# Performance work log

Hardware: AMD Instinct MI355X
Metric: run time of the kernel (lower is better)

## Reference

```python
import jax, jax.numpy as jnp
import numpy as np

B, L, D, K, NRBF = 2, 2048, 128, 3, 16
NUM_ATOMS = 118


def setup_inputs() -> dict:
    key = jax.random.key(0)
    ks = jax.random.split(key, 20)
    s = 0.05
    inp = {
        "coords": jax.random.normal(ks[0], (B, L, 3), dtype=jnp.float32) * 3.0,
        "Z": jax.random.randint(ks[1], (B, L), 0, NUM_ATOMS),
        # CoordEncoder params
        "atom_emb": jax.random.normal(ks[2], (NUM_ATOMS, D), dtype=jnp.float32) * s,
        "gamma": jnp.asarray(10.0, dtype=jnp.float32),
        "rbf_centers": jnp.linspace(0.0, 5.0, NRBF, dtype=jnp.float32),
        "rbf_w": jax.random.normal(ks[3], (NRBF, D), dtype=jnp.float32) * s,
        "rbf_b": jnp.zeros((D,), dtype=jnp.float32),
        "out_w": jax.random.normal(ks[4], (2 * D, D), dtype=jnp.float32) * s,
        "out_b": jnp.zeros((D,), dtype=jnp.float32),
        # MP_Layer params, stacked over K layers
        "self_w": jax.random.normal(ks[5], (K, D, D), dtype=jnp.float32) * s,
        "self_b": jnp.zeros((K, D), dtype=jnp.float32),
        "msg_w": jax.random.normal(ks[6], (K, D, D), dtype=jnp.float32) * s,
        "msg_b": jnp.zeros((K, D), dtype=jnp.float32),
        "upd_w": jax.random.normal(ks[7], (K, 2 * D, D), dtype=jnp.float32) * s,
        "upd_b": jnp.zeros((K, D), dtype=jnp.float32),
    }
    return inp


def _pairwise_dist(coords):
    # coords: [B,L,3] -> dist: [B,L,L]; safe sqrt so diagonal has zero grad
    diff = coords[:, :, None, :] - coords[:, None, :, :]
    sq = jnp.sum(diff * diff, axis=-1)
    return jnp.where(sq > 0, jnp.sqrt(jnp.where(sq > 0, sq, 1.0)), 0.0)


def reference(coords, Z, atom_emb, gamma, rbf_centers, rbf_w, rbf_b,
              out_w, out_b, self_w, self_b, msg_w, msg_b, upd_w, upd_b):
    # --- CoordEncoder ---
    h_atom = atom_emb[Z]                                   # [B,L,D]
    dist = _pairwise_dist(coords)                          # [B,L,L]
    rbf = jnp.exp(-gamma * (dist[..., None] - rbf_centers) ** 2)  # [B,L,L,R]
    rbf_local = rbf.mean(axis=2)                           # [B,L,R]
    h_geo = rbf_local @ rbf_w + rbf_b                      # [B,L,D]
    h = jnp.concatenate([h_atom, h_geo], axis=-1) @ out_w + out_b  # [B,L,D]
    # --- MP layers (mask is None; W = exp(-dist) is the same every layer) ---
    W = jnp.exp(-dist)                                     # [B,L,L]
    for k in range(K):
        msg = jnp.einsum("bij,bjd->bid", W, h @ msg_w[k] + msg_b[k])
        h = jnp.concatenate([h @ self_w[k] + self_b[k], msg], axis=-1) @ upd_w[k] + upd_b[k]
    return h
```

## Files before the change

### kernel.cpp

```cpp
#include <hip/hip_runtime.h>
#include <hip/hip_bf16.h>

typedef unsigned short u16;
typedef __bf16 bf16x8 __attribute__((ext_vector_type(8)));
typedef float f32x4 __attribute__((ext_vector_type(4)));
typedef u16 u16x4 __attribute__((ext_vector_type(4)));

#define B_ 2
#define L_ 2048
#define D_ 128
#define KLAY 3
#define NR 16
#define DD (D_ * D_)
#define XTN (L_ * D_)
#define NFOLD 6

static __device__ __forceinline__ u16 f2bf(float f) {
    union { float f; unsigned u; } v; v.f = f;
    unsigned r = v.u + 0x7FFFu + ((v.u >> 16) & 1u);
    return (u16)(r >> 16);
}
static __device__ __forceinline__ bf16x8 ld_bf8(const u16* p) {
    return *(const bf16x8*)p;
}

__global__ __launch_bounds__(1024) void enc_kernel(
    const float* coords, const int* Z, const float* atom_emb,
    const float* gamma_p, const float* centers, const float* rbf_w,
    const float* rbf_b, const float* out_w, const float* out_b,
    const float* self_w, const float* self_b, const float* msg_w,
    const float* msg_b, const float* upd_w, const float* upd_b,
    u16* h_rm, u16* hT, float* rowsum,
    u16* foldA, u16* foldB, float* c0v, float* cvv) {
    int bid = blockIdx.x;
    int tid = threadIdx.x;
    int w = tid >> 6, lane = tid & 63;
    int rowf = lane & 15, kg = lane >> 4;
    __shared__ __align__(16) char smem[34816];
    f32x4 z = {0.f, 0.f, 0.f, 0.f};

    if (bid < NFOLD) {
        int lay = bid >> 1, mat = bid & 1;
        const float* Wsrc = (mat ? msg_w : self_w) + lay * DD;
        const float* U = upd_w + lay * 2 * DD + mat * DD;
        u16* dst = (mat ? foldB : foldA) + lay * DD;
        u16(*A_l)[68] = (u16(*)[68])smem;
        u16(*BT_l)[68] = (u16(*)[68])(smem + 17408);
        f32x4 acc[4] = {z, z, z, z};
        int ncol = (w & 7) * 16 + rowf;
        int rfh = w >> 3;
        for (int half = 0; half < 2; half++) {
            int m0 = half * 64;
            for (int o = tid; o < 128 * 64; o += 1024) {
                int kk = o >> 6, mm = o & 63;
                A_l[kk][mm] = f2bf(Wsrc[kk * D_ + m0 + mm]);
            }
            for (int o = tid; o < 128 * 64; o += 1024) {
                int nn = o >> 6, mm = o & 63;
                BT_l[nn][mm] = f2bf(U[(m0 + mm) * D_ + nn]);
            }
            __syncthreads();
#pragma unroll
            for (int rfi = 0; rfi < 4; rfi++) {
                int rf = rfh * 4 + rfi;
#pragma unroll
                for (int ks = 0; ks < 2; ks++) {
                    int k0 = ks * 32 + kg * 8;
                    acc[rfi] = __builtin_amdgcn_mfma_f32_16x16x32_bf16(
                        ld_bf8(&A_l[rf * 16 + rowf][k0]),
                        ld_bf8(&BT_l[ncol][k0]), acc[rfi], 0, 0, 0);
                }
            }
            __syncthreads();
        }
#pragma unroll
        for (int rfi = 0; rfi < 4; rfi++) {
            int rf = rfh * 4 + rfi;
            u16x4 pk;
#pragma unroll
            for (int r = 0; r < 4; r++) pk[r] = f2bf(acc[rfi][r]);
            *(u16x4*)&dst[ncol * D_ + rf * 16 + kg * 4] = pk;
        }
        if (tid < D_) {
            const float* bsrc = (mat ? msg_b : self_b) + lay * D_;
            float s = 0.f;
            for (int m = 0; m < D_; m++) s += bsrc[m] * U[m * D_ + tid];
            if (mat == 0) c0v[lay * D_ + tid] = s + upd_b[lay * D_ + tid];
            else cvv[lay * D_ + tid] = s;
        }
        return;
    }

    int rt = bid - NFOLD;
    int gi0 = rt * 16;
    int b = gi0 >> 11;
    int il0 = gi0 & (L_ - 1);
    float* cj = (float*)smem;
    u16* hgeo = (u16*)(smem + 24576);
    float* rbf_l = (float*)(smem + 24576 + 4352);

    for (int i = tid; i < 1536; i += 1024)
        ((float4*)cj)[i] = ((const float4*)(coords + (size_t)b * L_ * 3))[i];
    __syncthreads();

    {
        int row = tid >> 6, s6 = tid & 63;
        float gamma = gamma_p[0];
        float dl = centers[1] - centers[0];
        float c4[4];
#pragma unroll
        for (int g = 0; g < 4; g++) c4[g] = centers[4 * g];
        float two_gdl = 2.f * gamma * dl;
        float cx = cj[(il0 + row) * 3 + 0];
        float cy = cj[(il0 + row) * 3 + 1];
        float cz = cj[(il0 + row) * 3 + 2];
        float acc[4][4];
#pragma unroll
        for (int g = 0; g < 4; g++)
#pragma unroll
            for (int m = 0; m < 4; m++) acc[g][m] = 0.f;
        float wsum = 0.f;
        for (int it = 0; it < 32; it++) {
            int j = s6 + 64 * it;
            float dx = cx - cj[j * 3 + 0];
            float dy = cy - cj[j * 3 + 1];
            float dz = cz - cj[j * 3 + 2];
            float sq = dx * dx + dy * dy + dz * dz;
            float d = sqrtf(sq);
            wsum += __expf(-d);
#pragma unroll
            for (int g = 0; g < 4; g++) {
                float x = d - c4[g];
                float base = __expf(-gamma * x * x);
                float u = __expf(fminf(two_gdl * x, 29.f));
                float p = base;
                acc[g][0] += p;
                p *= u; acc[g][1] += p;
                p *= u; acc[g][2] += p;
                p *= u; acc[g][3] += p;
            }
        }
#pragma unroll
        for (int off = 32; off > 0; off >>= 1) {
            wsum += __shfl_xor(wsum, off);
#pragma unroll
            for (int g = 0; g < 4; g++)
#pragma unroll
                for (int m = 0; m < 4; m++) acc[g][m] += __shfl_xor(acc[g][m], off);
        }
        if (s6 == 0) {
            rowsum[gi0 + row] = wsum;
#pragma unroll
            for (int m = 0; m < 4; m++) {
                float Km = __expf(-gamma * (m * dl) * (m * dl)) * (1.0f / L_);
#pragma unroll
                for (int g = 0; g < 4; g++)
                    rbf_l[row * NR + 4 * g + m] = acc[g][m] * Km;
            }
        }
    }
    __syncthreads();

    for (int e = tid; e < 16 * D_; e += 1024) {
        int row = e >> 7, d = e & 127;
        float s = rbf_b[d];
#pragma unroll
        for (int r = 0; r < NR; r++) s += rbf_l[row * NR + r] * rbf_w[r * D_ + d];
        hgeo[row * 136 + d] = f2bf(s);
    }
    __syncthreads();

    if (w < 8) {
        f32x4 a1 = z;
        int za = Z[gi0 + rowf];
        int cl = w * 16 + rowf;
#pragma unroll
        for (int ks = 0; ks < 8; ks++) {
            int k0 = ks * 32 + kg * 8;
            bf16x8 av;
            if (k0 < 128) {
                union { bf16x8 v; u16 e[8]; } t;
                const float* ap = atom_emb + (size_t)za * D_ + k0;
#pragma unroll
                for (int e = 0; e < 8; e++) t.e[e] = f2bf(ap[e]);
                av = t.v;
            } else {
                av = ld_bf8(hgeo + rowf * 136 + (k0 - 128));
            }
            union { bf16x8 v; u16 e[8]; } bv;
            const float* bp = out_w + (size_t)k0 * D_ + cl;
#pragma unroll
            for (int e = 0; e < 8; e++) bv.e[e] = f2bf(bp[e * D_]);
            a1 = __builtin_amdgcn_mfma_f32_16x16x32_bf16(av, bv.v, a1, 0, 0, 0);
        }
        float bias = out_b[cl];
        u16x4 pk;
#pragma unroll
        for (int r = 0; r < 4; r++) pk[r] = f2bf(a1[r] + bias);
#pragma unroll
        for (int r = 0; r < 4; r++)
            h_rm[(size_t)(gi0 + kg * 4 + r) * D_ + cl] = pk[r];
        *(u16x4*)&hT[(size_t)b * XTN + ((il0 + kg * 4) >> 5) * (32 * D_) + cl * 32 +
                     ((il0 + kg * 4) & 31)] = pk;
    }
}

__global__ __launch_bounds__(1024) void mp_kernel(
    const float* coords, const u16* h_in, const u16* hT_in, const float* rowsum,
    const u16* foldA_k, const u16* foldB_k, const float* c0_k, const float* cv_k,
    u16* h_out, u16* hT_out, float* out_f32, int last) {
    int rt = blockIdx.x;
    int gi0 = rt * 16;
    int b = gi0 >> 11;
    int il0 = gi0 & (L_ - 1);
    int tid = threadIdx.x;
    int w = tid >> 6, lane = tid & 63;
    int rowf = lane & 15, kg = lane >> 4;

    __shared__ __align__(16) float cj[L_ * 3];
    __shared__ __align__(16) float red[4][16][128];
    u16* g_lds = (u16*)&red[0][0][0];

    for (int i = tid; i < 1536; i += 1024)
        ((float4*)cj)[i] = ((const float4*)(coords + (size_t)b * L_ * 3))[i];
    __syncthreads();

    float rx = cj[(il0 + rowf) * 3 + 0];
    float ry = cj[(il0 + rowf) * 3 + 1];
    float rz = cj[(il0 + rowf) * 3 + 2];

    f32x4 z = {0.f, 0.f, 0.f, 0.f};
    f32x4 acc[8] = {z, z, z, z, z, z, z, z};
    const u16* xbase = hT_in + (size_t)b * XTN + (w * 4) * (32 * D_) + rowf * 32 + kg * 8;
#pragma unroll
    for (int s = 0; s < 4; s++) {
        int j0 = w * 128 + s * 32 + kg * 8;
        union { bf16x8 v; __bf16 e[8]; } wf;
#pragma unroll
        for (int e = 0; e < 8; e++) {
            int jl = j0 + e;
            float dx = rx - cj[jl * 3 + 0];
            float dy = ry - cj[jl * 3 + 1];
            float dz = rz - cj[jl * 3 + 2];
            float sq = dx * dx + dy * dy + dz * dz;
            float d = sq > 0.f ? sqrtf(sq) : 0.f;
            wf.e[e] = (__bf16)__expf(-d);
        }
#pragma unroll
        for (int n = 0; n < 8; n++) {
            bf16x8 bb = ld_bf8(xbase + s * (32 * D_) + n * 512);
            acc[n] = __builtin_amdgcn_mfma_f32_16x16x32_bf16(wf.v, bb, acc[n], 0, 0, 0);
        }
    }
    auto stash = [&](int slot) {
#pragma unroll
        for (int n = 0; n < 8; n++)
#pragma unroll
            for (int r = 0; r < 4; r++) {
                int row = kg * 4 + r, col = n * 16 + rowf;
                red[slot][row][(col + 4 * row) & 127] = acc[n][r];
            }
    };
    auto grab = [&](int slot) {
#pragma unroll
        for (int n = 0; n < 8; n++)
#pragma unroll
            for (int r = 0; r < 4; r++) {
                int row = kg * 4 + r, col = n * 16 + rowf;
                acc[n][r] += red[slot][row][(col + 4 * row) & 127];
            }
    };
    if (w >= 8 && w < 12) stash(w - 8);
    __syncthreads();
    if (w < 4) grab(w);
    __syncthreads();
    if (w >= 12) stash(w - 12);
    __syncthreads();
    if (w >= 4 && w < 8) grab(w - 4);
    __syncthreads();
    if (w >= 4 && w < 8) stash(w - 4);
    __syncthreads();
    if (w < 4) grab(w);
    if (w == 2 || w == 3) stash(w);
    __syncthreads();
    if (w < 2) grab(w + 2);
    if (w == 1) stash(3);
    __syncthreads();
    if (w == 0) {
        grab(3);
#pragma unroll
        for (int n = 0; n < 8; n++)
#pragma unroll
            for (int r = 0; r < 4; r++)
                g_lds[(kg * 4 + r) * 136 + n * 16 + rowf] = f2bf(acc[n][r]);
    }
    __syncthreads();

    if (w < 8) {
        f32x4 acc2 = z;
        int cl = w * 16 + rowf;
#pragma unroll
        for (int ks = 0; ks < 4; ks++) {
            int k0 = ks * 32 + kg * 8;
            bf16x8 ah = ld_bf8(h_in + (size_t)(gi0 + rowf) * D_ + k0);
            acc2 = __builtin_amdgcn_mfma_f32_16x16x32_bf16(
                ah, ld_bf8(foldA_k + cl * D_ + k0), acc2, 0, 0, 0);
            bf16x8 ag = ld_bf8(g_lds + rowf * 136 + k0);
            acc2 = __builtin_amdgcn_mfma_f32_16x16x32_bf16(
                ag, ld_bf8(foldB_k + cl * D_ + k0), acc2, 0, 0, 0);
        }
        float c0 = c0_k[cl], cv = cv_k[cl];
        if (last) {
#pragma unroll
            for (int r = 0; r < 4; r++) {
                int row = kg * 4 + r;
                out_f32[(size_t)(gi0 + row) * D_ + cl] =
                    acc2[r] + c0 + rowsum[gi0 + row] * cv;
            }
        } else {
#pragma unroll
            for (int r = 0; r < 4; r++) {
                int row = kg * 4 + r;
                float val = acc2[r] + c0 + rowsum[gi0 + row] * cv;
                u16 hv = f2bf(val);
                h_out[(size_t)(gi0 + row) * D_ + cl] = hv;
                int jj = il0 + row;
                hT_out[(size_t)b * XTN + (jj >> 5) * (32 * D_) + cl * 32 + (jj & 31)] = hv;
            }
        }
    }
}

extern "C" void kernel_launch(void* const* d_in, const int* in_sizes, int n_in,
                              void* d_out, int out_size, void* d_ws, size_t ws_size,
                              hipStream_t stream) {
    const float* coords = (const float*)d_in[0];
    const int* Z = (const int*)d_in[1];
    const float* atom_emb = (const float*)d_in[2];
    const float* gamma = (const float*)d_in[3];
    const float* centers = (const float*)d_in[4];
    const float* rbf_w = (const float*)d_in[5];
    const float* rbf_b = (const float*)d_in[6];
    const float* out_w = (const float*)d_in[7];
    const float* out_b = (const float*)d_in[8];
    const float* self_w = (const float*)d_in[9];
    const float* self_b = (const float*)d_in[10];
    const float* msg_w = (const float*)d_in[11];
    const float* msg_b = (const float*)d_in[12];
    const float* upd_w = (const float*)d_in[13];
    const float* upd_b = (const float*)d_in[14];
    float* out = (float*)d_out;

    char* ws = (char*)d_ws;
    u16* h_a = (u16*)(ws + 0);
    u16* h_b = (u16*)(ws + 1048576);
    u16* hT_a = (u16*)(ws + 2097152);
    u16* hT_b = (u16*)(ws + 3145728);
    float* rowsum = (float*)(ws + 4194304);
    u16* foldA = (u16*)(ws + 4210688);
    u16* foldB = (u16*)(ws + 4308992);
    float* c0v = (float*)(ws + 4407296);
    float* cvv = (float*)(ws + 4408832);

    enc_kernel<<<256 + NFOLD, 1024, 0, stream>>>(
        coords, Z, atom_emb, gamma, centers, rbf_w, rbf_b, out_w, out_b,
        self_w, self_b, msg_w, msg_b, upd_w, upd_b,
        h_a, hT_a, rowsum, foldA, foldB, c0v, cvv);
    mp_kernel<<<256, 1024, 0, stream>>>(
        coords, h_a, hT_a, rowsum, foldA + 0 * DD, foldB + 0 * DD,
        c0v + 0 * D_, cvv + 0 * D_, h_b, hT_b, out, 0);
    mp_kernel<<<256, 1024, 0, stream>>>(
        coords, h_b, hT_b, rowsum, foldA + 1 * DD, foldB + 1 * DD,
        c0v + 1 * D_, cvv + 1 * D_, h_a, hT_a, out, 0);
    mp_kernel<<<256, 1024, 0, stream>>>(
        coords, h_a, hT_a, rowsum, foldA + 2 * DD, foldB + 2 * DD,
        c0v + 2 * D_, cvv + 2 * D_, h_b, hT_b, out, 1);
}
```

Baseline: 109.2 us.

## Split encoder into pairwise partial-sum kernel and finalize kernel with j-split

The fused encoder kernel becomes two kernels. The first computes pairwise RBF and exp(-d) partial sums, with each 16-row tile's j-range split into 4 quarter blocks (1024 blocks of 512 threads). The second reduces the partials and runs the rbf_w and out_w projections. The aim is more parallelism and occupancy for the dominant pairwise stage, which had only 256 large blocks. The cost is an extra launch plus a global-memory round trip for the partial sums. The weight-fold blocks also change to 512 threads, each computing 8 output tiles.

```diff
diff --git a/kernel.cpp b/kernel.cpp
--- a/kernel.cpp
+++ b/kernel.cpp
@@ -13,6 +13,8 @@
 #define NR 16
 #define DD (D_ * D_)
 #define XTN (L_ * D_)
+#define BL (B_ * L_)
+#define BLN (BL * NR)
 #define NFOLD 6
 
 static __device__ __forceinline__ u16 f2bf(float f) {
@@ -24,62 +26,55 @@
     return *(const bf16x8*)p;
 }
 
-__global__ __launch_bounds__(1024) void enc_kernel(
-    const float* coords, const int* Z, const float* atom_emb,
-    const float* gamma_p, const float* centers, const float* rbf_w,
-    const float* rbf_b, const float* out_w, const float* out_b,
-    const float* self_w, const float* self_b, const float* msg_w,
-    const float* msg_b, const float* upd_w, const float* upd_b,
-    u16* h_rm, u16* hT, float* rowsum,
-    u16* foldA, u16* foldB, float* c0v, float* cvv) {
+__global__ __launch_bounds__(512) void pairw_kernel(
+    const float* coords, const float* gamma_p, const float* centers,
+    const float* self_w, const float* msg_w, const float* upd_w,
+    const float* self_b, const float* msg_b, const float* upd_b,
+    float* rbfp, float* rsp, u16* foldA, u16* foldB, float* c0v, float* cvv) {
     int bid = blockIdx.x;
     int tid = threadIdx.x;
-    int w = tid >> 6, lane = tid & 63;
-    int rowf = lane & 15, kg = lane >> 4;
     __shared__ __align__(16) char smem[34816];
     f32x4 z = {0.f, 0.f, 0.f, 0.f};
 
     if (bid < NFOLD) {
+        int w = tid >> 6, lane = tid & 63;
+        int rowf = lane & 15, kg = lane >> 4;
         int lay = bid >> 1, mat = bid & 1;
         const float* Wsrc = (mat ? msg_w : self_w) + lay * DD;
         const float* U = upd_w + lay * 2 * DD + mat * DD;
         u16* dst = (mat ? foldB : foldA) + lay * DD;
         u16(*A_l)[68] = (u16(*)[68])smem;
         u16(*BT_l)[68] = (u16(*)[68])(smem + 17408);
-        f32x4 acc[4] = {z, z, z, z};
-        int ncol = (w & 7) * 16 + rowf;
-        int rfh = w >> 3;
+        f32x4 acc[8] = {z, z, z, z, z, z, z, z};
         for (int half = 0; half < 2; half++) {
             int m0 = half * 64;
-            for (int o = tid; o < 128 * 64; o += 1024) {
+            for (int o = tid; o < 128 * 64; o += 512) {
                 int kk = o >> 6, mm = o & 63;
                 A_l[kk][mm] = f2bf(Wsrc[kk * D_ + m0 + mm]);
             }
-            for (int o = tid; o < 128 * 64; o += 1024) {
+            for (int o = tid; o < 128 * 64; o += 512) {
                 int nn = o >> 6, mm = o & 63;
                 BT_l[nn][mm] = f2bf(U[(m0 + mm) * D_ + nn]);
             }
             __syncthreads();
 #pragma unroll
-            for (int rfi = 0; rfi < 4; rfi++) {
-                int rf = rfh * 4 + rfi;
+            for (int rf = 0; rf < 8; rf++)
 #pragma unroll
                 for (int ks = 0; ks < 2; ks++) {
                     int k0 = ks * 32 + kg * 8;
-                    acc[rfi] = __builtin_amdgcn_mfma_f32_16x16x32_bf16(
+                    acc[rf] = __builtin_amdgcn_mfma_f32_16x16x32_bf16(
                         ld_bf8(&A_l[rf * 16 + rowf][k0]),
-                        ld_bf8(&BT_l[ncol][k0]), acc[rfi], 0, 0, 0);
+                        ld_bf8(&BT_l[w * 16 + rowf][k0]), acc[rf], 0, 0, 0);
                 }
-            }
             __syncthreads();
         }
-#pragma unroll
-        for (int rfi = 0; rfi < 4; rfi++) {
-            int rf = rfh * 4 + rfi;
+        int n = w * 16 + rowf;
+#pragma unroll
+        for (int rf = 0; rf < 8; rf++) {
             u16x4 pk;
 #pragma unroll
-            for (int r = 0; r < 4; r++) pk[r] = f2bf(acc[rfi][r]);
-            *(u16x4*)&dst[ncol * D_ + rf * 16 + kg * 4] = pk;
+            for (int r = 0; r < 4; r++) pk[r] = f2bf(acc[rf][r]);
+            *(u16x4*)&dst[n * D_ + rf * 16 + kg * 4] = pk;
         }
         if (tid < D_) {
             const float* bsrc = (mat ? msg_b : self_b) + lay * D_;
@@ -91,89 +86,117 @@
         return;
     }
 
-    int rt = bid - NFOLD;
+    int rt = (bid - NFOLD) >> 2, jq = (bid - NFOLD) & 3;
     int gi0 = rt * 16;
     int b = gi0 >> 11;
+    int row = tid >> 5, s5 = tid & 31;
+    int gi = gi0 + row;
+    float* cj = (float*)smem;
+    {
+        const float4* src = (const float4*)(coords + ((size_t)b * L_ + jq * 512) * 3);
+        if (tid < 384) ((float4*)cj)[tid] = src[tid];
+    }
+    float gamma = gamma_p[0];
+    float dl = centers[1] - centers[0];
+    float c4[4];
+#pragma unroll
+    for (int g = 0; g < 4; g++) c4[g] = centers[4 * g];
+    float two_gdl = 2.f * gamma * dl;
+    float cx = coords[gi * 3 + 0];
+    float cy = coords[gi * 3 + 1];
+    float cz = coords[gi * 3 + 2];
+    __syncthreads();
+
+    float acc[4][4];
+#pragma unroll
+    for (int g = 0; g < 4; g++)
+#pragma unroll
+        for (int m = 0; m < 4; m++) acc[g][m] = 0.f;
+    float wsum = 0.f;
+#pragma unroll 4
+    for (int it = 0; it < 16; it++) {
+        int jl = s5 + 32 * it;
+        float dx = cx - cj[jl * 3 + 0];
+        float dy = cy - cj[jl * 3 + 1];
+        float dz = cz - cj[jl * 3 + 2];
+        float sq = dx * dx + dy * dy + dz * dz;
+        float d = sqrtf(sq);
+        wsum += __expf(-d);
+#pragma unroll
+        for (int g = 0; g < 4; g++) {
+            float x = d - c4[g];
+            float base = __expf(-gamma * x * x);
+            float u1 = __expf(fminf(two_gdl * x, 29.f));
+            float u2 = u1 * u1;
+            acc[g][0] += base;
+            acc[g][1] += base * u1;
+            acc[g][2] += base * u2;
+            acc[g][3] += base * (u2 * u1);
+        }
+    }
+#pragma unroll
+    for (int off = 16; off > 0; off >>= 1) {
+        wsum += __shfl_xor(wsum, off);
+#pragma unroll
+        for (int g = 0; g < 4; g++)
+#pragma unroll
+            for (int m = 0; m < 4; m++) acc[g][m] += __shfl_xor(acc[g][m], off);
+    }
+    if (s5 == 0) {
+        rsp[(size_t)jq * BL + gi] = wsum;
+#pragma unroll
+        for (int m = 0; m < 4; m++) {
+            float Km = __expf(-gamma * (m * dl) * (m * dl)) * (1.0f / L_);
+#pragma unroll
+            for (int g = 0; g < 4; g++)
+                rbfp[(size_t)jq * BLN + (size_t)gi * NR + 4 * g + m] = acc[g][m] * Km;
+        }
+    }
+}
+
+__global__ __launch_bounds__(256) void encf_kernel(
+    const int* Z, const float* atom_emb, const float* rbf_w, const float* rbf_b,
+    const float* out_w, const float* out_b, const float* rbfp, const float* rsp,
+    u16* h_rm, u16* hT, float* rowsum) {
+    int gi0 = blockIdx.x * 16;
+    int b = gi0 >> 11;
     int il0 = gi0 & (L_ - 1);
-    float* cj = (float*)smem;
-    u16* hgeo = (u16*)(smem + 24576);
-    float* rbf_l = (float*)(smem + 24576 + 4352);
-
-    for (int i = tid; i < 1536; i += 1024)
-        ((float4*)cj)[i] = ((const float4*)(coords + (size_t)b * L_ * 3))[i];
-    __syncthreads();
+    int tid = threadIdx.x;
+    int w = tid >> 6, lane = tid & 63;
+    int rowf = lane & 15, kg = lane >> 4;
+    __shared__ float rbf_lds[16][NR];
+    __shared__ __align__(16) u16 hgeo[16][136];
 
     {
-        int row = tid >> 6, s6 = tid & 63;
-        float gamma = gamma_p[0];
-        float dl = centers[1] - centers[0];
-        float c4[4];
-#pragma unroll
-        for (int g = 0; g < 4; g++) c4[g] = centers[4 * g];
-        float two_gdl = 2.f * gamma * dl;
-        float cx = cj[(il0 + row) * 3 + 0];
-        float cy = cj[(il0 + row) * 3 + 1];
-        float cz = cj[(il0 + row) * 3 + 2];
-        float acc[4][4];
-#pragma unroll
-        for (int g = 0; g < 4; g++)
-#pragma unroll
-            for (int m = 0; m < 4; m++) acc[g][m] = 0.f;
-        float wsum = 0.f;
-        for (int it = 0; it < 32; it++) {
-            int j = s6 + 64 * it;
-            float dx = cx - cj[j * 3 + 0];
-            float dy = cy - cj[j * 3 + 1];
-            float dz = cz - cj[j * 3 + 2];
-            float sq = dx * dx + dy * dy + dz * dz;
-            float d = sqrtf(sq);
-            wsum += __expf(-d);
-#pragma unroll
-            for (int g = 0; g < 4; g++) {
-                float x = d - c4[g];
-                float base = __expf(-gamma * x * x);
-                float u = __expf(fminf(two_gdl * x, 29.f));
-                float p = base;
-                acc[g][0] += p;
-                p *= u; acc[g][1] += p;
-                p *= u; acc[g][2] += p;
-                p *= u; acc[g][3] += p;
-            }
-        }
-#pragma unroll
-        for (int off = 32; off > 0; off >>= 1) {
-            wsum += __shfl_xor(wsum, off);
-#pragma unroll
-            for (int g = 0; g < 4; g++)
-#pragma unroll
-                for (int m = 0; m < 4; m++) acc[g][m] += __shfl_xor(acc[g][m], off);
-        }
-        if (s6 == 0) {
-            rowsum[gi0 + row] = wsum;
-#pragma unroll
-            for (int m = 0; m < 4; m++) {
-                float Km = __expf(-gamma * (m * dl) * (m * dl)) * (1.0f / L_);
-#pragma unroll
-                for (int g = 0; g < 4; g++)
-                    rbf_l[row * NR + 4 * g + m] = acc[g][m] * Km;
-            }
-        }
-    }
-    __syncthreads();
-
-    for (int e = tid; e < 16 * D_; e += 1024) {
+        int row = tid >> 4, r = tid & 15;
+        float s = 0.f;
+#pragma unroll
+        for (int p = 0; p < 4; p++)
+            s += rbfp[(size_t)p * BLN + (size_t)(gi0 + row) * NR + r];
+        rbf_lds[row][r] = s;
+    }
+    if (tid < 16) {
+        float s = 0.f;
+#pragma unroll
+        for (int p = 0; p < 4; p++) s += rsp[(size_t)p * BL + gi0 + tid];
+        rowsum[gi0 + tid] = s;
+    }
+    __syncthreads();
+    for (int e = tid; e < 16 * D_; e += 256) {
         int row = e >> 7, d = e & 127;
         float s = rbf_b[d];
 #pragma unroll
-        for (int r = 0; r < NR; r++) s += rbf_l[row * NR + r] * rbf_w[r * D_ + d];
-        hgeo[row * 136 + d] = f2bf(s);
-    }
-    __syncthreads();
-
-    if (w < 8) {
+        for (int r = 0; r < NR; r++) s += rbf_lds[row][r] * rbf_w[r * D_ + d];
+        hgeo[row][d] = f2bf(s);
+    }
+    __syncthreads();
+
+    f32x4 z = {0.f, 0.f, 0.f, 0.f};
+    int za = Z[gi0 + rowf];
+#pragma unroll
+    for (int q = 0; q < 2; q++) {
+        int cl = (w * 2 + q) * 16 + rowf;
         f32x4 a1 = z;
-        int za = Z[gi0 + rowf];
-        int cl = w * 16 + rowf;
 #pragma unroll
         for (int ks = 0; ks < 8; ks++) {
             int k0 = ks * 32 + kg * 8;
@@ -185,7 +208,7 @@
                 for (int e = 0; e < 8; e++) t.e[e] = f2bf(ap[e]);
                 av = t.v;
             } else {
-                av = ld_bf8(hgeo + rowf * 136 + (k0 - 128));
+                av = ld_bf8(&hgeo[rowf][k0 - 128]);
             }
             union { bf16x8 v; u16 e[8]; } bv;
             const float* bp = out_w + (size_t)k0 * D_ + cl;
@@ -200,8 +223,8 @@
 #pragma unroll
         for (int r = 0; r < 4; r++)
             h_rm[(size_t)(gi0 + kg * 4 + r) * D_ + cl] = pk[r];
-        *(u16x4*)&hT[(size_t)b * XTN + ((il0 + kg * 4) >> 5) * (32 * D_) + cl * 32 +
-                     ((il0 + kg * 4) & 31)] = pk;
+        int jj = il0 + kg * 4;
+        *(u16x4*)&hT[(size_t)b * XTN + (jj >> 5) * (32 * D_) + cl * 32 + (jj & 31)] = pk;
     }
 }
 
@@ -361,11 +384,14 @@
     u16* foldB = (u16*)(ws + 4308992);
     float* c0v = (float*)(ws + 4407296);
     float* cvv = (float*)(ws + 4408832);
-
-    enc_kernel<<<256 + NFOLD, 1024, 0, stream>>>(
-        coords, Z, atom_emb, gamma, centers, rbf_w, rbf_b, out_w, out_b,
-        self_w, self_b, msg_w, msg_b, upd_w, upd_b,
-        h_a, hT_a, rowsum, foldA, foldB, c0v, cvv);
+    float* rbfp = (float*)(ws + 4410368);
+    float* rsp = (float*)(ws + 5458944);
+
+    pairw_kernel<<<NFOLD + 1024, 512, 0, stream>>>(
+        coords, gamma, centers, self_w, msg_w, upd_w, self_b, msg_b, upd_b,
+        rbfp, rsp, foldA, foldB, c0v, cvv);
+    encf_kernel<<<256, 256, 0, stream>>>(
+        Z, atom_emb, rbf_w, rbf_b, out_w, out_b, rbfp, rsp, h_a, hT_a, rowsum);
     mp_kernel<<<256, 1024, 0, stream>>>(
         coords, h_a, hT_a, rowsum, foldA + 0 * DD, foldB + 0 * DD,
         c0v + 0 * D_, cvv + 0 * D_, h_b, hT_b, out, 0);
```

Result: faster. 98.27 us (-10.0%).
